# Optimization experiments

Hardware: AMD Instinct MI355X
Metric: run time of the kernel (lower is better)

## Reference

```python
import jax, jax.numpy as jnp
import numpy as np

N_NODES = 50000
N_EDGES = 800000
D_IN = 128
HIDDEN = 64
N_CLASSES = 2


def gcn_conv(x, edge_index, W, b, num_nodes):
    """PyG GCNConv: linear (no bias) -> add self-loops -> sym-normalized aggregate -> + bias."""
    h = x @ W  # [N, H]
    loop = jnp.arange(num_nodes, dtype=edge_index.dtype)
    src = jnp.concatenate([edge_index[0], loop])  # [E+N]
    dst = jnp.concatenate([edge_index[1], loop])
    deg = jax.ops.segment_sum(jnp.ones_like(dst, dtype=h.dtype), dst, num_segments=num_nodes)
    dinv = jnp.where(deg > 0, jax.lax.rsqrt(deg), 0.0)
    norm = dinv[src] * dinv[dst]  # [E+N]
    msg = h[src] * norm[:, None]  # [E+N, H]  (gather + scale)
    out = jax.ops.segment_sum(msg, dst, num_segments=num_nodes)  # scatter-add
    return out + b


def setup_inputs() -> dict:
    key = jax.random.key(0)
    ks = jax.random.split(key, 6)
    x = jax.random.normal(ks[0], (N_NODES, D_IN), dtype=jnp.float32)
    edge_index = jax.random.randint(ks[1], (2, N_EDGES), 0, N_NODES, dtype=jnp.int64)
    # Glorot-ish init for weights, zero bias (PyG default)
    W1 = jax.random.normal(ks[2], (D_IN, HIDDEN), dtype=jnp.float32) * (1.0 / np.sqrt(D_IN))
    b1 = jnp.zeros((HIDDEN,), dtype=jnp.float32)
    W2 = jax.random.normal(ks[3], (HIDDEN, N_CLASSES), dtype=jnp.float32) * (1.0 / np.sqrt(HIDDEN))
    b2 = jnp.zeros((N_CLASSES,), dtype=jnp.float32)
    return {"x": x, "edge_index": edge_index, "W1": W1, "b1": b1, "W2": W2, "b2": b2}


def reference(x, edge_index, W1, b1, W2, b2):
    h = jax.nn.relu(gcn_conv(x, edge_index, W1, b1, N_NODES))
    # F.dropout(training=self.training) is identity in eval mode
    out = gcn_conv(h, edge_index, W2, b2, N_NODES)
    return out
```

## Files before the change

### kernel.cpp

```cpp
#include <hip/hip_runtime.h>

#define N_NODES 50000
#define N_EDGES 800000
#define D_IN 128
#define HIDDEN 64
#define N_CLASSES 2
#define NBUK 782
#define NBUK_P 784
#define NBLK 196
#define NBLK_P 200
#define NE4 200000
#define XPAD 136

typedef _Float16 half4v __attribute__((ext_vector_type(4)));
typedef _Float16 h8 __attribute__((ext_vector_type(8)));
typedef float f4 __attribute__((ext_vector_type(4)));


__global__ __launch_bounds__(256) void k_hist(const int4* __restrict__ dst4,
                                              int* __restrict__ bhist) {
    __shared__ int hist[NBUK];
    int t = threadIdx.x;
    for (int i = t; i < NBUK; i += 256) hist[i] = 0;
    __syncthreads();
    int base4 = blockIdx.x * 1024;
#pragma unroll
    for (int k = 0; k < 4; k++) {
        int idx = base4 + k * 256 + t;
        if (idx < NE4) {
            int4 d = dst4[idx];
            atomicAdd(&hist[d.x >> 6], 1);
            atomicAdd(&hist[d.y >> 6], 1);
            atomicAdd(&hist[d.z >> 6], 1);
            atomicAdd(&hist[d.w >> 6], 1);
        }
    }
    __syncthreads();
    for (int i = t; i < NBUK; i += 256) bhist[blockIdx.x * NBUK_P + i] = hist[i];
}


__global__ __launch_bounds__(256) void k_colscan(const int* __restrict__ bhist,
                                                 int* __restrict__ excT,
                                                 int* __restrict__ colsum) {
    __shared__ int part[256];
    int b = blockIdx.x;
    int t = threadIdx.x;
    int v = (t < NBLK) ? bhist[t * NBUK_P + b] : 0;
    part[t] = v;
    __syncthreads();
    for (int off = 1; off < 256; off <<= 1) {
        int p = (t >= off) ? part[t - off] : 0;
        __syncthreads();
        part[t] += p;
        __syncthreads();
    }
    if (t < NBLK) excT[b * NBLK_P + t] = part[t] - v;
    if (t == 255) colsum[b] = part[255];
}


__global__ __launch_bounds__(256) void k_binA2s(const int4* __restrict__ src4,
                                                const int4* __restrict__ dst4,
                                                const int* __restrict__ excT,
                                                const int* __restrict__ colsum,
                                                int* __restrict__ bucket_off,
                                                int* __restrict__ row_ptr,
                                                int* __restrict__ ebin) {
    __shared__ int part[256];
    __shared__ int cur[NBUK];
    const int b = blockIdx.x;
    const int t = threadIdx.x;

    int v[4];
    int s = 0;
#pragma unroll
    for (int i = 0; i < 4; i++) {
        int idx = t * 4 + i;
        v[i] = (idx < NBUK) ? colsum[idx] : 0;
        s += v[i];
    }
    part[t] = s;
    __syncthreads();
    for (int off = 1; off < 256; off <<= 1) {
        int p = (t >= off) ? part[t - off] : 0;
        __syncthreads();
        part[t] += p;
        __syncthreads();
    }
    int run = (t == 0) ? 0 : part[t - 1];
#pragma unroll
    for (int i = 0; i < 4; i++) {
        int idx = t * 4 + i;
        if (idx < NBUK) {
            cur[idx] = run + excT[idx * NBLK_P + b];
            if (b == 0) bucket_off[idx] = run;
            run += v[i];
        } else if (idx == NBUK && b == 0) {
            bucket_off[idx] = run;
        }
    }
    if (b == 0 && t == 0) row_ptr[N_NODES] = N_EDGES;
    __syncthreads();

    int base4 = b * 1024;
#pragma unroll
    for (int k = 0; k < 4; k++) {
        int idx = base4 + k * 256 + t;
        if (idx < NE4) {
            int4 sv = src4[idx];
            int4 d = dst4[idx];
            int p0 = atomicAdd(&cur[d.x >> 6], 1);
            int p1 = atomicAdd(&cur[d.y >> 6], 1);
            int p2 = atomicAdd(&cur[d.z >> 6], 1);
            int p3 = atomicAdd(&cur[d.w >> 6], 1);
            ebin[p0] = (sv.x << 7) | (d.x & 63);
            ebin[p1] = (sv.y << 7) | (d.y & 63);
            ebin[p2] = (sv.z << 7) | (d.z & 63);
            ebin[p3] = (sv.w << 7) | (d.w & 63);
        }
    }
}


__global__ __launch_bounds__(256) void k_csr_gemm(
    const int* __restrict__ ebin, const int* __restrict__ bucket_off,
    const float* __restrict__ x, const float* __restrict__ W1,
    int* __restrict__ row_ptr, float* __restrict__ dinv_g,
    int* __restrict__ rec, _Float16* __restrict__ hs)
{
    __shared__ _Float16 xs[64 * XPAD];
    __shared__ _Float16 Wt[64 * XPAD];
    __shared__ int cnt[64];
    __shared__ int cur[64];
    __shared__ float sdinv[64];
    const int b = blockIdx.x;
    const int t = threadIdx.x;
    const int row0 = b * 64;

    for (int i4 = t; i4 < 64 * D_IN / 4; i4 += 256) {
        int r = i4 >> 5;
        int k4 = (i4 & 31) << 2;
        int grow = row0 + r;
        half4v hv;
        if (grow < N_NODES) {
            float4 v = *(const float4*)&x[grow * D_IN + k4];
            hv.x = (_Float16)v.x; hv.y = (_Float16)v.y;
            hv.z = (_Float16)v.z; hv.w = (_Float16)v.w;
        } else {
            hv.x = hv.y = hv.z = hv.w = (_Float16)0.f;
        }
        *(half4v*)&xs[r * XPAD + k4] = hv;
    }
    for (int i4 = t; i4 < D_IN * HIDDEN / 4; i4 += 256) {
        float4 v = *(const float4*)&W1[i4 * 4];
        int k = i4 >> 4;
        int n = (i4 & 15) << 2;
        Wt[(n + 0) * XPAD + k] = (_Float16)v.x;
        Wt[(n + 1) * XPAD + k] = (_Float16)v.y;
        Wt[(n + 2) * XPAD + k] = (_Float16)v.z;
        Wt[(n + 3) * XPAD + k] = (_Float16)v.w;
    }

    if (t < 64) cnt[t] = 0;
    __syncthreads();
    int beg = bucket_off[b], end = bucket_off[b + 1];
    for (int i = beg + t; i < end; i += 256) atomicAdd(&cnt[ebin[i] & 63], 1);
    __syncthreads();
    if (t < 64) {
        int deg = cnt[t];
        int sum = deg;
#pragma unroll
        for (int off = 1; off < 64; off <<= 1) {
            int v = __shfl_up(sum, off, 64);
            if (t >= off) sum += v;
        }
        int rp = beg + sum - deg;
        cur[t] = rp;
        float di = rsqrtf((float)(deg + 1));
        sdinv[t] = di;
        int node = row0 + t;
        if (node < N_NODES) {
            row_ptr[node] = rp;
            dinv_g[node] = di;
        }
    }
    __syncthreads();
    for (int i = beg + t; i < end; i += 256) {
        int pk = ebin[i];
        int pos = atomicAdd(&cur[pk & 63], 1);
        rec[pos] = pk >> 7;
    }
    __syncthreads();

    const int w = t >> 6;
    const int L = t & 63;
    const int mrow = w * 16 + (L & 15);
    const int qk = (L >> 4) * 8;
    f4 acc0 = {0.f, 0.f, 0.f, 0.f}, acc1 = acc0, acc2 = acc0, acc3 = acc0;
#pragma unroll
    for (int ks = 0; ks < D_IN; ks += 32) {
        h8 a = *(const h8*)&xs[mrow * XPAD + ks + qk];
        h8 b0 = *(const h8*)&Wt[(0 * 16 + (L & 15)) * XPAD + ks + qk];
        h8 b1 = *(const h8*)&Wt[(1 * 16 + (L & 15)) * XPAD + ks + qk];
        h8 b2 = *(const h8*)&Wt[(2 * 16 + (L & 15)) * XPAD + ks + qk];
        h8 b3 = *(const h8*)&Wt[(3 * 16 + (L & 15)) * XPAD + ks + qk];
        acc0 = __builtin_amdgcn_mfma_f32_16x16x32_f16(a, b0, acc0, 0, 0, 0);
        acc1 = __builtin_amdgcn_mfma_f32_16x16x32_f16(a, b1, acc1, 0, 0, 0);
        acc2 = __builtin_amdgcn_mfma_f32_16x16x32_f16(a, b2, acc2, 0, 0, 0);
        acc3 = __builtin_amdgcn_mfma_f32_16x16x32_f16(a, b3, acc3, 0, 0, 0);
    }

    const int n0 = L & 15;
#pragma unroll
    for (int j = 0; j < 4; j++) {
        int m = w * 16 + (L >> 4) * 4 + j;
        float di = sdinv[m];
        size_t base = (size_t)(row0 + m) * HIDDEN;
        hs[base + 0 * 16 + n0] = (_Float16)(acc0[j] * di);
        hs[base + 1 * 16 + n0] = (_Float16)(acc1[j] * di);
        hs[base + 2 * 16 + n0] = (_Float16)(acc2[j] * di);
        hs[base + 3 * 16 + n0] = (_Float16)(acc3[j] * di);
    }
}


__global__ __launch_bounds__(256) void k_agg1_l2(
    const _Float16* __restrict__ hs, const int* __restrict__ row_ptr,
    const int* __restrict__ rec, const float* __restrict__ dinv,
    const float* __restrict__ b1, const float* __restrict__ W2,
    float* __restrict__ zs)
{
    const int node = blockIdx.x * 16 + (threadIdx.x >> 4);
    const int g = threadIdx.x & 15;
    const int gbase = threadIdx.x & 48;
    const half4v* H = (const half4v*)hs;

    float di = dinv[node];
    float4 acc = make_float4(0.f, 0.f, 0.f, 0.f);

    int beg = row_ptr[node];
    int end = row_ptr[node + 1];

    for (int base = beg; base < end; base += 16) {
        int n = end - base;
        if (n > 16) n = 16;
        int r = N_NODES;
        if (g < n) r = rec[base + g];
        int n8 = (n + 7) & ~7;
        for (int e = 0; e < n8; e += 8) {
            int i0 = gbase + e;
            int s0 = __shfl(r, i0 + 0, 64);
            int s1 = __shfl(r, i0 + 1, 64);
            int s2 = __shfl(r, i0 + 2, 64);
            int s3 = __shfl(r, i0 + 3, 64);
            int s4 = __shfl(r, i0 + 4, 64);
            int s5 = __shfl(r, i0 + 5, 64);
            int s6 = __shfl(r, i0 + 6, 64);
            int s7 = __shfl(r, i0 + 7, 64);
            half4v a0 = H[s0 * 16 + g];
            half4v a1 = H[s1 * 16 + g];
            half4v a2 = H[s2 * 16 + g];
            half4v a3 = H[s3 * 16 + g];
            half4v a4 = H[s4 * 16 + g];
            half4v a5 = H[s5 * 16 + g];
            half4v a6 = H[s6 * 16 + g];
            half4v a7 = H[s7 * 16 + g];
            acc.x += ((float)a0.x + (float)a1.x) + ((float)a2.x + (float)a3.x)
                   + ((float)a4.x + (float)a5.x) + ((float)a6.x + (float)a7.x);
            acc.y += ((float)a0.y + (float)a1.y) + ((float)a2.y + (float)a3.y)
                   + ((float)a4.y + (float)a5.y) + ((float)a6.y + (float)a7.y);
            acc.z += ((float)a0.z + (float)a1.z) + ((float)a2.z + (float)a3.z)
                   + ((float)a4.z + (float)a5.z) + ((float)a6.z + (float)a7.z);
            acc.w += ((float)a0.w + (float)a1.w) + ((float)a2.w + (float)a3.w)
                   + ((float)a4.w + (float)a5.w) + ((float)a6.w + (float)a7.w);
        }
    }

    half4v sv = H[node * 16 + g];
    acc.x += (float)sv.x;
    acc.y += (float)sv.y;
    acc.z += (float)sv.z;
    acc.w += (float)sv.w;

    float4 bb = ((const float4*)b1)[g];
    float4 y;
    y.x = fmaxf(fmaf(acc.x, di, bb.x), 0.f);
    y.y = fmaxf(fmaf(acc.y, di, bb.y), 0.f);
    y.z = fmaxf(fmaf(acc.z, di, bb.z), 0.f);
    y.w = fmaxf(fmaf(acc.w, di, bb.w), 0.f);
    float4 wA = ((const float4*)W2)[2 * g];
    float4 wB = ((const float4*)W2)[2 * g + 1];
    float p0 = y.x * wA.x + y.y * wA.z + y.z * wB.x + y.w * wB.z;
    float p1 = y.x * wA.y + y.y * wA.w + y.z * wB.y + y.w * wB.w;

    p0 += __shfl_down(p0, 8, 64);
    p1 += __shfl_down(p1, 8, 64);
    p0 += __shfl_down(p0, 4, 64);
    p1 += __shfl_down(p1, 4, 64);
    p0 += __shfl_down(p0, 2, 64);
    p1 += __shfl_down(p1, 2, 64);
    p0 += __shfl_down(p0, 1, 64);
    p1 += __shfl_down(p1, 1, 64);
    if (g == 0) {
        zs[node * 2 + 0] = p0 * di;
        zs[node * 2 + 1] = p1 * di;
    }
}


__global__ __launch_bounds__(256) void k_agg2(
    const float* __restrict__ zs, const int* __restrict__ row_ptr,
    const int* __restrict__ rec, const float* __restrict__ dinv,
    const float* __restrict__ b2, float* __restrict__ out)
{
    const int node = blockIdx.x * 32 + (threadIdx.x >> 3);
    const int j = threadIdx.x & 7;
    if (node >= N_NODES) return;
    int beg = row_ptr[node];
    int end = row_ptr[node + 1];
    float a0 = 0.f, a1 = 0.f;
    for (int idx = beg + j; idx < end; idx += 8) {
        int s = rec[idx];
        float2 v = *(const float2*)&zs[s * 2];
        a0 += v.x;
        a1 += v.y;
    }
    a0 += __shfl_down(a0, 4, 64);
    a1 += __shfl_down(a1, 4, 64);
    a0 += __shfl_down(a0, 2, 64);
    a1 += __shfl_down(a1, 2, 64);
    a0 += __shfl_down(a0, 1, 64);
    a1 += __shfl_down(a1, 1, 64);
    if (j == 0) {
        float di = dinv[node];
        float2 zv = *(const float2*)&zs[node * 2];
        float2 o;
        o.x = fmaf(di, a0 + zv.x, b2[0]);
        o.y = fmaf(di, a1 + zv.y, b2[1]);
        *(float2*)&out[node * 2] = o;
    }
}


extern "C" void kernel_launch(void* const* d_in, const int* in_sizes, int n_in,
                              void* d_out, int out_size, void* d_ws, size_t ws_size,
                              hipStream_t stream) {
    const float* x  = (const float*)d_in[0];
    const int* ei   = (const int*)d_in[1];
    const float* W1 = (const float*)d_in[2];
    const float* b1 = (const float*)d_in[3];
    const float* W2 = (const float*)d_in[4];
    const float* b2 = (const float*)d_in[5];
    float* out = (float*)d_out;

    const int4* src4 = (const int4*)ei;
    const int4* dst4 = (const int4*)(ei + N_EDGES);

    int*      bucket_off = (int*)d_ws;
    int*      colsum     = (int*)d_ws + 1024;
    float*    dinv       = (float*)d_ws + 2048;
    int*      row_ptr    = (int*)d_ws + 52224;
    int*      bhist      = (int*)d_ws + 102432;
    int*      excT       = (int*)d_ws + 256128;
    int*      ebin       = (int*)d_ws + 412576;
    int*      rec        = (int*)d_ws + 1212576;
    _Float16* hs         = (_Float16*)((int*)d_ws + 2012576);
    float*    zs         = (float*)d_ws + 3614112;

    k_hist<<<NBLK, 256, 0, stream>>>(dst4, bhist);
    k_colscan<<<NBUK, 256, 0, stream>>>(bhist, excT, colsum);
    k_binA2s<<<NBLK, 256, 0, stream>>>(src4, dst4, excT, colsum, bucket_off, row_ptr, ebin);
    k_csr_gemm<<<NBUK, 256, 0, stream>>>(ebin, bucket_off, x, W1, row_ptr, dinv, rec, hs);
    k_agg1_l2<<<N_NODES / 16, 256, 0, stream>>>(hs, row_ptr, rec, dinv, b1, W2, zs);
    k_agg2<<<(N_NODES + 31) / 32, 256, 0, stream>>>(zs, row_ptr, rec, dinv, b2, out);
}
```

Baseline: 128.3 us.

## Use 8-lane nodes with 16-byte fp16 gathers in layer-1 aggregation; nontemporal edge traffic

The layer-1 aggregation kernel now assigns 8 lanes per node, each loading 8 halves (16 bytes) per neighbor row, so each block covers 32 nodes instead of 16. The loop processes 8 edges per step and drops the inner 16-edge chunking. Wider loads should cut the instruction count per gathered row, and more nodes per wave should improve latency hiding. Separately, the ebin and rec writes and reads are marked nontemporal to keep them from polluting cache; this risks losing L2 reuse, since rec is read again by both aggregation kernels.

```diff
diff --git a/kernel.cpp b/kernel.cpp
--- a/kernel.cpp
+++ b/kernel.cpp
@@ -114,10 +114,10 @@
             int p1 = atomicAdd(&cur[d.y >> 6], 1);
             int p2 = atomicAdd(&cur[d.z >> 6], 1);
             int p3 = atomicAdd(&cur[d.w >> 6], 1);
-            ebin[p0] = (sv.x << 7) | (d.x & 63);
-            ebin[p1] = (sv.y << 7) | (d.y & 63);
-            ebin[p2] = (sv.z << 7) | (d.z & 63);
-            ebin[p3] = (sv.w << 7) | (d.w & 63);
+            __builtin_nontemporal_store((sv.x << 7) | (d.x & 63), &ebin[p0]);
+            __builtin_nontemporal_store((sv.y << 7) | (d.y & 63), &ebin[p1]);
+            __builtin_nontemporal_store((sv.z << 7) | (d.z & 63), &ebin[p2]);
+            __builtin_nontemporal_store((sv.w << 7) | (d.w & 63), &ebin[p3]);
         }
     }
 }
@@ -189,7 +189,7 @@
     for (int i = beg + t; i < end; i += 256) {
         int pk = ebin[i];
         int pos = atomicAdd(&cur[pk & 63], 1);
-        rec[pos] = pk >> 7;
+        __builtin_nontemporal_store(pk >> 7, &rec[pos]);
     }
     __syncthreads();
 
@@ -231,71 +231,64 @@
     const float* __restrict__ b1, const float* __restrict__ W2,
     float* __restrict__ zs)
 {
-    const int node = blockIdx.x * 16 + (threadIdx.x >> 4);
-    const int g = threadIdx.x & 15;
-    const int gbase = threadIdx.x & 48;
-    const half4v* H = (const half4v*)hs;
+    const int node = blockIdx.x * 32 + (threadIdx.x >> 3);
+    const int g = threadIdx.x & 7;
+    const int gbase = threadIdx.x & 56;
+    if (node >= N_NODES) return;
+    const h8* H = (const h8*)hs;
 
     float di = dinv[node];
-    float4 acc = make_float4(0.f, 0.f, 0.f, 0.f);
+    float acc[8];
+#pragma unroll
+    for (int i = 0; i < 8; i++) acc[i] = 0.f;
 
     int beg = row_ptr[node];
     int end = row_ptr[node + 1];
 
-    for (int base = beg; base < end; base += 16) {
+    for (int base = beg; base < end; base += 8) {
         int n = end - base;
-        if (n > 16) n = 16;
+        if (n > 8) n = 8;
         int r = N_NODES;
-        if (g < n) r = rec[base + g];
-        int n8 = (n + 7) & ~7;
-        for (int e = 0; e < n8; e += 8) {
-            int i0 = gbase + e;
-            int s0 = __shfl(r, i0 + 0, 64);
-            int s1 = __shfl(r, i0 + 1, 64);
-            int s2 = __shfl(r, i0 + 2, 64);
-            int s3 = __shfl(r, i0 + 3, 64);
-            int s4 = __shfl(r, i0 + 4, 64);
-            int s5 = __shfl(r, i0 + 5, 64);
-            int s6 = __shfl(r, i0 + 6, 64);
-            int s7 = __shfl(r, i0 + 7, 64);
-            half4v a0 = H[s0 * 16 + g];
-            half4v a1 = H[s1 * 16 + g];
-            half4v a2 = H[s2 * 16 + g];
-            half4v a3 = H[s3 * 16 + g];
-            half4v a4 = H[s4 * 16 + g];
-            half4v a5 = H[s5 * 16 + g];
-            half4v a6 = H[s6 * 16 + g];
-            half4v a7 = H[s7 * 16 + g];
-            acc.x += ((float)a0.x + (float)a1.x) + ((float)a2.x + (float)a3.x)
-                   + ((float)a4.x + (float)a5.x) + ((float)a6.x + (float)a7.x);
-            acc.y += ((float)a0.y + (float)a1.y) + ((float)a2.y + (float)a3.y)
-                   + ((float)a4.y + (float)a5.y) + ((float)a6.y + (float)a7.y);
-            acc.z += ((float)a0.z + (float)a1.z) + ((float)a2.z + (float)a3.z)
-                   + ((float)a4.z + (float)a5.z) + ((float)a6.z + (float)a7.z);
-            acc.w += ((float)a0.w + (float)a1.w) + ((float)a2.w + (float)a3.w)
-                   + ((float)a4.w + (float)a5.w) + ((float)a6.w + (float)a7.w);
-        }
-    }
-
-    half4v sv = H[node * 16 + g];
-    acc.x += (float)sv.x;
-    acc.y += (float)sv.y;
-    acc.z += (float)sv.z;
-    acc.w += (float)sv.w;
-
-    float4 bb = ((const float4*)b1)[g];
-    float4 y;
-    y.x = fmaxf(fmaf(acc.x, di, bb.x), 0.f);
-    y.y = fmaxf(fmaf(acc.y, di, bb.y), 0.f);
-    y.z = fmaxf(fmaf(acc.z, di, bb.z), 0.f);
-    y.w = fmaxf(fmaf(acc.w, di, bb.w), 0.f);
-    float4 wA = ((const float4*)W2)[2 * g];
-    float4 wB = ((const float4*)W2)[2 * g + 1];
-    float p0 = y.x * wA.x + y.y * wA.z + y.z * wB.x + y.w * wB.z;
-    float p1 = y.x * wA.y + y.y * wA.w + y.z * wB.y + y.w * wB.w;
-
-    p0 += __shfl_down(p0, 8, 64);
-    p1 += __shfl_down(p1, 8, 64);
+        if (g < n) r = __builtin_nontemporal_load(&rec[base + g]);
+        int s0 = __shfl(r, gbase + 0, 64);
+        int s1 = __shfl(r, gbase + 1, 64);
+        int s2 = __shfl(r, gbase + 2, 64);
+        int s3 = __shfl(r, gbase + 3, 64);
+        int s4 = __shfl(r, gbase + 4, 64);
+        int s5 = __shfl(r, gbase + 5, 64);
+        int s6 = __shfl(r, gbase + 6, 64);
+        int s7 = __shfl(r, gbase + 7, 64);
+        h8 a0 = H[s0 * 8 + g];
+        h8 a1 = H[s1 * 8 + g];
+        h8 a2 = H[s2 * 8 + g];
+        h8 a3 = H[s3 * 8 + g];
+        h8 a4 = H[s4 * 8 + g];
+        h8 a5 = H[s5 * 8 + g];
+        h8 a6 = H[s6 * 8 + g];
+        h8 a7 = H[s7 * 8 + g];
+#pragma unroll
+        for (int i = 0; i < 8; i++) {
+            acc[i] += ((float)a0[i] + (float)a1[i]) + ((float)a2[i] + (float)a3[i])
+                    + ((float)a4[i] + (float)a5[i]) + ((float)a6[i] + (float)a7[i]);
+        }
+    }
+
+    h8 sv = H[node * 8 + g];
+#pragma unroll
+    for (int i = 0; i < 8; i++) acc[i] += (float)sv[i];
+
+    f4 bbA = ((const f4*)b1)[2 * g];
+    f4 bbB = ((const f4*)b1)[2 * g + 1];
+    float p0 = 0.f, p1 = 0.f;
+#pragma unroll
+    for (int i = 0; i < 8; i++) {
+        float bb = (i < 4) ? bbA[i] : bbB[i - 4];
+        float y = fmaxf(fmaf(acc[i], di, bb), 0.f);
+        float2 w2 = *(const float2*)&W2[(8 * g + i) * N_CLASSES];
+        p0 = fmaf(y, w2.x, p0);
+        p1 = fmaf(y, w2.y, p1);
+    }
+
     p0 += __shfl_down(p0, 4, 64);
     p1 += __shfl_down(p1, 4, 64);
     p0 += __shfl_down(p0, 2, 64);
@@ -321,7 +314,7 @@
     int end = row_ptr[node + 1];
     float a0 = 0.f, a1 = 0.f;
     for (int idx = beg + j; idx < end; idx += 8) {
-        int s = rec[idx];
+        int s = __builtin_nontemporal_load(&rec[idx]);
         float2 v = *(const float2*)&zs[s * 2];
         a0 += v.x;
         a1 += v.y;
@@ -372,6 +365,6 @@
     k_colscan<<<NBUK, 256, 0, stream>>>(bhist, excT, colsum);
     k_binA2s<<<NBLK, 256, 0, stream>>>(src4, dst4, excT, colsum, bucket_off, row_ptr, ebin);
     k_csr_gemm<<<NBUK, 256, 0, stream>>>(ebin, bucket_off, x, W1, row_ptr, dinv, rec, hs);
-    k_agg1_l2<<<N_NODES / 16, 256, 0, stream>>>(hs, row_ptr, rec, dinv, b1, W2, zs);
+    k_agg1_l2<<<(N_NODES + 31) / 32, 256, 0, stream>>>(hs, row_ptr, rec, dinv, b1, W2, zs);
     k_agg2<<<(N_NODES + 31) / 32, 256, 0, stream>>>(zs, row_ptr, rec, dinv, b2, out);
 }
```

After: 146.9 us. 14.5% more time.
